# Performance work log

Hardware: AMD Instinct MI355X
Metric: run time of the kernel (lower is better)

Reference implementation:

```python
import jax, jax.numpy as jnp
import numpy as np

N1 = 10000; N2 = 10000; F_IN = 256
E_EDGES = 480000; P_PAIRS = 200000
HID = 128; H = 8; DH = 16; L = 2


def _segment_softmax(logits, seg, n):
    # softmax over edges sharing the same destination node (per head)
    m = jax.ops.segment_max(logits, seg, num_segments=n)
    m = jnp.where(jnp.isfinite(m), m, 0.0)
    e = jnp.exp(logits - m[seg])
    s = jax.ops.segment_sum(e, seg, num_segments=n)
    return e / (s[seg] + 1e-16)


def _attend(q_dst, k_src, v_src, src, dst, arel, mrel, prior, n_dst):
    # q_dst: [Nd,H,D]; k_src/v_src: [Ns,H,D]; arel/mrel: [H,D,D]; prior: [H]
    k = jnp.einsum('nhd,hde->nhe', k_src, arel)[src]   # [E,H,D]
    v = jnp.einsum('nhd,hde->nhe', v_src, mrel)[src]   # [E,H,D]
    logits = jnp.einsum('ehd,ehd->eh', q_dst[dst], k) * prior / jnp.sqrt(jnp.asarray(DH, q_dst.dtype))
    a = _segment_softmax(logits, dst, n_dst)           # [E,H]
    out = jax.ops.segment_sum(a[..., None] * v, dst, num_segments=n_dst)
    return out.reshape(n_dst, HID)


def _forward(x_n1, x_n2, Win1, bin1, Win2, bin2, Wk, bk, Wq, bq, Wv, bv, Wa, ba, skip, arel, mrel, prior, ei12, ei21, edge_index):
    proj = lambda x, W, b: (x @ W + b).reshape(-1, H, DH)
    h1 = jax.nn.relu(x_n1 @ Win1 + bin1)
    h2 = jax.nn.relu(x_n2 @ Win2 + bin2)
    feats1, feats2 = [], []
    for l in range(L):
        k1, q1, v1 = proj(h1, Wk[l, 0], bk[l, 0]), proj(h1, Wq[l, 0], bq[l, 0]), proj(h1, Wv[l, 0], bv[l, 0])
        k2, q2, v2 = proj(h2, Wk[l, 1], bk[l, 1]), proj(h2, Wq[l, 1], bq[l, 1]), proj(h2, Wv[l, 1], bv[l, 1])
        # edge type 0: n1 -> n2 (dst = n2); edge type 1: n2 -> n1 (dst = n1)
        agg2 = _attend(q2, k1, v1, ei12[0], ei12[1], arel[l, 0], mrel[l, 0], prior[l, 0], N2)
        agg1 = _attend(q1, k2, v2, ei21[0], ei21[1], arel[l, 1], mrel[l, 1], prior[l, 1], N1)
        o1 = jax.nn.gelu(agg1) @ Wa[l, 0] + ba[l, 0]
        o2 = jax.nn.gelu(agg2) @ Wa[l, 1] + ba[l, 1]
        s1 = jax.nn.sigmoid(skip[l, 0]); s2 = jax.nn.sigmoid(skip[l, 1])
        h1 = s1 * o1 + (1.0 - s1) * h1
        h2 = s2 * o2 + (1.0 - s2) * h2
        feats1.append(h1); feats2.append(h2)
    Em = jnp.concatenate(feats1, axis=1)   # [N1, HID*L]
    Ed = jnp.concatenate(feats2, axis=1)   # [N2, HID*L]
    # scores = Em @ Ed.T then gather at (m_index, d_index); computed as gathered dot
    # products (same math, avoids [N1,N2] materialization). Dropout in eval mode.
    preds = jnp.einsum('pc,pc->p', Em[edge_index[0]], Ed[edge_index[1]])[:, None]
    return preds


def setup_inputs():
    key = jax.random.key(0)
    ks = jax.random.split(key, 16)
    sc = 0.05
    inp = {}
    inp['x_n1'] = jax.random.normal(ks[0], (N1, F_IN), jnp.float32)
    inp['x_n2'] = jax.random.normal(ks[1], (N2, F_IN), jnp.float32)
    inp['ei12'] = jnp.stack([jax.random.randint(ks[2], (E_EDGES,), 0, N1),
                             jax.random.randint(ks[3], (E_EDGES,), 0, N2)])
    inp['ei21'] = jnp.stack([jax.random.randint(ks[4], (E_EDGES,), 0, N2),
                             jax.random.randint(ks[5], (E_EDGES,), 0, N1)])
    inp['edge_index'] = jnp.stack([jax.random.randint(ks[6], (P_PAIRS,), 0, N1),
                                   jax.random.randint(ks[7], (P_PAIRS,), 0, N2)])
    inp['Win1'] = jax.random.normal(ks[8], (F_IN, HID), jnp.float32) * sc
    inp['bin1'] = jnp.zeros((HID,), jnp.float32)
    inp['Win2'] = jax.random.normal(ks[9], (F_IN, HID), jnp.float32) * sc
    inp['bin2'] = jnp.zeros((HID,), jnp.float32)
    inp['Wk'] = jax.random.normal(ks[10], (L, 2, HID, HID), jnp.float32) * sc
    inp['bk'] = jnp.zeros((L, 2, HID), jnp.float32)
    inp['Wq'] = jax.random.normal(ks[11], (L, 2, HID, HID), jnp.float32) * sc
    inp['bq'] = jnp.zeros((L, 2, HID), jnp.float32)
    inp['Wv'] = jax.random.normal(ks[12], (L, 2, HID, HID), jnp.float32) * sc
    inp['bv'] = jnp.zeros((L, 2, HID), jnp.float32)
    inp['Wa'] = jax.random.normal(ks[13], (L, 2, HID, HID), jnp.float32) * sc
    inp['ba'] = jnp.zeros((L, 2, HID), jnp.float32)
    inp['skip'] = jnp.ones((L, 2), jnp.float32)
    inp['arel'] = jax.random.normal(ks[14], (L, 2, H, DH, DH), jnp.float32) * 0.25
    inp['mrel'] = jax.random.normal(ks[15], (L, 2, H, DH, DH), jnp.float32) * 0.25
    inp['prior'] = jnp.ones((L, 2, H), jnp.float32)
    return inp


def reference(x_n1, x_n2, ei12, ei21, edge_index, Win1, bin1, Win2, bin2, Wk, bk, Wq, bq, Wv, bv, Wa, ba, skip, arel, mrel, prior):
    return _forward(x_n1, x_n2, Win1, bin1, Win2, bin2, Wk, bk, Wq, bq, Wv, bv, Wa, ba, skip, arel, mrel, prior, ei12, ei21, edge_index)
```

## Files before the change

### kernel.cpp

```cpp
#include <hip/hip_runtime.h>
#include <math.h>

#define N1c 10000
#define N2c 10000
#define F_INc 256
#define Ec 480000
#define Pc 200000
#define Lc 2
#define NPART 32
#define NPc 313
#define NBLK 256
#define CAPE 17408
#define CAPP 7936

using short8 = __attribute__((ext_vector_type(8))) short;
using float4v = __attribute__((ext_vector_type(4))) float;
using floatx2 = __attribute__((ext_vector_type(2))) float;

__device__ __forceinline__ float gelu_f(float x) {
    const float k0 = 0.7978845608028654f;
    const float k1 = 0.044715f;
    float x3 = x * x * x;
    float t = tanhf(k0 * (x + k1 * x3));
    return 0.5f * x * (1.0f + t);
}

__device__ __forceinline__ float bf2f(unsigned short x) {
    union { unsigned int u; float f; } c;
    c.u = ((unsigned int)x) << 16;
    return c.f;
}
__device__ __forceinline__ unsigned short f2bf(float f) {
    union { float f; unsigned int u; } c;
    c.f = f;
    unsigned int u = c.u;
    unsigned int r = (u + 0x7FFFu + ((u >> 16) & 1u)) >> 16;
    return (unsigned short)r;
}
__device__ __forceinline__ unsigned char f2fp8(float v) {
    unsigned int p = __builtin_amdgcn_cvt_pk_fp8_f32(v, v, 0u, false);
    return (unsigned char)(p & 0xFF);
}

__global__ __launch_bounds__(256) void prep_kernel(
    const float* __restrict__ Wq, const float* __restrict__ bq,
    const float* __restrict__ Wk, const float* __restrict__ bk,
    const float* __restrict__ Wv, const float* __restrict__ bv,
    const float* __restrict__ arel, const float* __restrict__ mrel,
    const float* __restrict__ prior,
    const float* __restrict__ Win1, const float* __restrict__ Win2,
    const float* __restrict__ Wa,
    short* __restrict__ Wqkvt, float* __restrict__ bqkv,
    short* __restrict__ Wint1, short* __restrict__ Wint2, short* __restrict__ Wat)
{
    int id = blockIdx.x * 256 + threadIdx.x;
    if (id < 196608) {
        int lt = id / 49152;
        int r = id - lt * 49152;
        int col = r >> 7, c = r & 127;
        short* Wout = Wqkvt + (size_t)lt * 384 * 128;
        float* bout = bqkv + lt * 384;
        if (col < 128) {
            Wout[col * 128 + c] = (short)f2bf(Wq[lt * 16384 + c * 128 + col]);
            if (c == 0) bout[col] = bq[lt * 128 + col];
            return;
        }
        int which = (col < 256) ? 0 : 1;
        int he = col - (which ? 256 : 128);
        int h = he >> 4, e = he & 15;
        const float* W = (which == 0 ? Wk : Wv) + lt * 16384;
        const float* b = (which == 0 ? bk : bv) + lt * 128;
        const float* R = (which == 0 ? arel : mrel) + lt * 2048;
        float sc = (which == 0) ? prior[lt * 8 + h] * 0.25f : 1.0f;
        float acc = 0.f;
        #pragma unroll
        for (int d = 0; d < 16; d++)
            acc += W[c * 128 + h * 16 + d] * R[(h * 16 + d) * 16 + e];
        Wout[col * 128 + c] = (short)f2bf(acc * sc);
        if (c == 0) {
            float bacc = 0.f;
            #pragma unroll
            for (int d = 0; d < 16; d++)
                bacc += b[h * 16 + d] * R[(h * 16 + d) * 16 + e];
            bout[col] = bacc * sc;
        }
    } else {
        int wid = id - 196608;
        if (wid < 65536) {
            int y = wid >> 15;
            int id2 = wid & 32767;
            int n = id2 >> 8, k = id2 & 255;
            const float* W = y ? Win2 : Win1;
            short* O = y ? Wint2 : Wint1;
            O[n * 256 + k] = (short)f2bf(W[k * 128 + n]);
        } else {
            int wid2 = wid - 65536;
            int lt = wid2 >> 14;
            int id2 = wid2 & 16383;
            int n = id2 >> 7, k = id2 & 127;
            Wat[lt * 16384 + n * 128 + k] = (short)f2bf(Wa[lt * 16384 + k * 128 + n]);
        }
    }
}

__global__ __launch_bounds__(256) void scatter_bins_kernel(
    const int* __restrict__ ei12, const int* __restrict__ ei21, const int* __restrict__ eidx,
    int* __restrict__ gcnt,
    unsigned int* __restrict__ stg12, unsigned int* __restrict__ stg21,
    unsigned int* __restrict__ stgm)
{
    int blk = blockIdx.x, z = blockIdx.y, t = threadIdx.x;
    const int* key; const int* pay; int E; unsigned int* stg; int cap;
    if (z == 0)      { key = ei12 + Ec; pay = ei12; E = Ec; stg = stg12; cap = CAPE; }
    else if (z == 1) { key = ei21 + Ec; pay = ei21; E = Ec; stg = stg21; cap = CAPE; }
    else             { key = eidx;      pay = nullptr; E = Pc; stg = stgm; cap = CAPP; }
    int chunk = (E + NBLK - 1) / NBLK;
    int start = blk * chunk;
    int stop = min(start + chunk, E);
    __shared__ int cnt[NPART];
    __shared__ int base[NPART];
    __shared__ int fill[NPART];
    if (t < NPART) cnt[t] = 0;
    __syncthreads();
    for (int e = start + t; e < stop; e += 256)
        atomicAdd(&cnt[key[e] / NPc], 1);
    __syncthreads();
    if (t < NPART) {
        base[t] = cnt[t] ? atomicAdd(&gcnt[z * NPART + t], cnt[t]) : 0;
        fill[t] = 0;
    }
    __syncthreads();
    for (int e = start + t; e < stop; e += 256) {
        unsigned int k = (unsigned int)key[e];
        int p = (int)(k / NPc);
        int r = atomicAdd(&fill[p], 1);
        unsigned int pk = (z == 2) ? ((k << 18) | (unsigned int)e)
                                   : ((k << 14) | (unsigned int)pay[e]);
        stg[(size_t)p * cap + base[p] + r] = pk;
    }
}

__global__ __launch_bounds__(256) void build_csr_kernel(
    const int* __restrict__ gcnt,
    const unsigned int* __restrict__ stg12, const unsigned int* __restrict__ stg21,
    const unsigned int* __restrict__ stgm,
    int* __restrict__ rp12, int* __restrict__ rp21, int* __restrict__ rpm,
    int* __restrict__ es12, int* __restrict__ es21, int* __restrict__ ps)
{
    int p = blockIdx.x, z = blockIdx.y, t = threadIdx.x;
    const unsigned int* stg; int* rowptr; int* out; int cap;
    if (z == 0)      { stg = stg12; rowptr = rp12; out = es12; cap = CAPE; }
    else if (z == 1) { stg = stg21; rowptr = rp21; out = es21; cap = CAPE; }
    else             { stg = stgm;  rowptr = rpm;  out = ps;   cap = CAPP; }
    int ksh = (z == 2) ? 18 : 14;
    unsigned int pmask = (z == 2) ? 0x3FFFFu : 0x3FFFu;
    int baseOut = 0, cntP = 0;
    #pragma unroll
    for (int j = 0; j < NPART; j++) {
        int c = gcnt[z * NPART + j];
        if (j < p) baseOut += c;
        if (j == p) cntP = c;
    }
    const unsigned int* sbase = stg + (size_t)p * cap;
    int lo = p * NPc;
    int hi = min(lo + NPc, 10000);

    __shared__ int hist[512];
    __shared__ int fill[NPc];
    hist[t] = 0; hist[t + 256] = 0;
    __syncthreads();
    for (int i = t; i < cntP; i += 256)
        atomicAdd(&hist[(int)(sbase[i] >> ksh) - lo], 1);
    __syncthreads();
    for (int off = 1; off < 512; off <<= 1) {
        int i0 = t, i1 = t + 256;
        int v0 = (i0 >= off) ? hist[i0 - off] : 0;
        int v1 = (i1 >= off) ? hist[i1 - off] : 0;
        __syncthreads();
        hist[i0] += v0; hist[i1] += v1;
        __syncthreads();
    }
    for (int i = t; i < NPc; i += 256) {
        int excl = i ? hist[i - 1] : 0;
        fill[i] = excl;
        if (lo + i < hi) rowptr[lo + i] = baseOut + excl;
    }
    if (p == NPART - 1 && t == 0) rowptr[10000] = baseOut + cntP;
    __syncthreads();
    for (int i = t; i < cntP; i += 256) {
        unsigned int pk = sbase[i];
        int r = atomicAdd(&fill[(int)(pk >> ksh) - lo], 1);
        out[baseOut + r] = (int)(pk & pmask);
    }
}

template<int A_GELU, int OUT_RELU, int SKIP, int PACKQKV, int ABF, int KT>
__global__ __launch_bounds__(256) void gemm_mfma(
    const void* __restrict__ A0v, const void* __restrict__ A1v, int ldA,
    const short* __restrict__ Wt0, const short* __restrict__ Wt1,
    const float* __restrict__ b0, const float* __restrict__ b1,
    unsigned short* __restrict__ C0, unsigned short* __restrict__ C1, int ldC,
    unsigned char* __restrict__ KV8o0, unsigned char* __restrict__ KV8o1,
    int M,
    const float* __restrict__ sk0, const float* __restrict__ sk1,
    const unsigned short* __restrict__ H0, const unsigned short* __restrict__ H1, int ldH)
{
    int z = blockIdx.z;
    const void* Av = z ? A1v : A0v;
    const short* Wt = z ? Wt1 : Wt0;
    const float* bias = z ? b1 : b0;
    unsigned short* C = z ? C1 : C0;
    unsigned char* KV8o = z ? KV8o1 : KV8o0;
    const float* skipv = z ? sk1 : sk0;
    const unsigned short* Hold = z ? H1 : H0;

    __shared__ short Alds[64 * 40];
    __shared__ short Blds[64 * 40];

    int tid = threadIdx.x;
    int w = tid >> 6;
    int l = tid & 63;
    int mBase = blockIdx.x * 64;
    int nBase = blockIdx.y * 64;

    int srow = tid >> 2;
    int koct = tid & 3;

    float4v acc[4];
    #pragma unroll
    for (int i = 0; i < 4; i++) acc[i] = (float4v){0.f, 0.f, 0.f, 0.f};

    int arow = mBase + srow;
    const short* Wptr = Wt + (size_t)(nBase + srow) * KT + koct * 8;

    int fl = l & 15;
    int fo = (l >> 4) * 8;

    #pragma unroll
    for (int k0 = 0; k0 < KT; k0 += 32) {
        uint4 raw;
        if (ABF) {
            const unsigned short* Ab = (const unsigned short*)Av;
            raw = make_uint4(0u, 0u, 0u, 0u);
            if (arow < M) raw = *(const uint4*)(Ab + (size_t)arow * ldA + k0 + koct * 8);
            if (A_GELU) {
                unsigned int wd[4] = {raw.x, raw.y, raw.z, raw.w};
                #pragma unroll
                for (int i = 0; i < 4; i++) {
                    float lo = gelu_f(bf2f((unsigned short)(wd[i] & 0xFFFFu)));
                    float hi = gelu_f(bf2f((unsigned short)(wd[i] >> 16)));
                    wd[i] = (unsigned int)f2bf(lo) | ((unsigned int)f2bf(hi) << 16);
                }
                raw = make_uint4(wd[0], wd[1], wd[2], wd[3]);
            }
        } else {
            const float* Af = (const float*)Av;
            float av[8];
            if (arow < M) {
                const float4* p = (const float4*)(Af + (size_t)arow * ldA + k0 + koct * 8);
                float4 f0 = p[0], f1 = p[1];
                av[0]=f0.x; av[1]=f0.y; av[2]=f0.z; av[3]=f0.w;
                av[4]=f1.x; av[5]=f1.y; av[6]=f1.z; av[7]=f1.w;
            } else {
                #pragma unroll
                for (int i = 0; i < 8; i++) av[i] = 0.f;
            }
            unsigned int pk[4];
            #pragma unroll
            for (int i = 0; i < 4; i++)
                pk[i] = (unsigned int)f2bf(av[2*i]) | ((unsigned int)f2bf(av[2*i+1]) << 16);
            raw = make_uint4(pk[0], pk[1], pk[2], pk[3]);
        }
        *(uint4*)&Alds[srow * 40 + koct * 8] = raw;
        *(uint4*)&Blds[srow * 40 + koct * 8] = *(const uint4*)(Wptr + k0);
        __syncthreads();

        short8 bfr = *(const short8*)&Blds[(w * 16 + fl) * 40 + fo];
        #pragma unroll
        for (int msub = 0; msub < 4; msub++) {
            short8 afr = *(const short8*)&Alds[(msub * 16 + fl) * 40 + fo];
            acc[msub] = __builtin_amdgcn_mfma_f32_16x16x32_bf16(afr, bfr, acc[msub], 0, 0, 0);
        }
        __syncthreads();
    }

    float sig = 0.f;
    if (SKIP) sig = 1.f / (1.f + __expf(-skipv[0]));
    int col = nBase + w * 16 + fl;
    float bcol = bias[col];
    int rbase = mBase + ((l >> 4) * 4);
    #pragma unroll
    for (int msub = 0; msub < 4; msub++) {
        #pragma unroll
        for (int r = 0; r < 4; r++) {
            int row = rbase + msub * 16 + r;
            if (row >= M) continue;
            float v = acc[msub][r] + bcol;
            if (OUT_RELU) v = fmaxf(v, 0.f);
            if (SKIP) v = sig * v + (1.f - sig) * bf2f(Hold[(size_t)row * ldH + col]);
            if (PACKQKV) {
                if (col < 128) {
                    C[(size_t)row * ldC + col] = f2bf(v);
                } else if (col < 256) {
                    int c = col - 128;
                    KV8o[(size_t)row * 256 + (c >> 3) * 16 + (c & 7)] = f2fp8(v);
                } else {
                    int c = col - 256;
                    KV8o[(size_t)row * 256 + (c >> 3) * 16 + 8 + (c & 7)] = f2fp8(v);
                }
            } else {
                C[(size_t)row * ldC + col] = f2bf(v);
            }
        }
    }
}

__global__ __launch_bounds__(128) void attend_kernel(
    const unsigned short* __restrict__ Qb1, const unsigned char* __restrict__ KV81,
    const unsigned short* __restrict__ Qb2, const unsigned char* __restrict__ KV82,
    const int* __restrict__ rp12, const int* __restrict__ es12,
    const int* __restrict__ rp21, const int* __restrict__ es21,
    unsigned short* __restrict__ agg1, unsigned short* __restrict__ agg2)
{
    int b = blockIdx.x;
    const unsigned short* Qb; const unsigned char* KV; const int* rp; const int* es;
    unsigned short* outb; int n;
    if (b < 1250) { n = b * 8 + (threadIdx.x >> 4);          Qb = Qb2; KV = KV81; rp = rp12; es = es12; outb = agg2; }
    else          { n = (b - 1250) * 8 + (threadIdx.x >> 4); Qb = Qb1; KV = KV82; rp = rp21; es = es21; outb = agg1; }
    int ln = threadIdx.x & 15;

    float q[8];
    {
        const ushort4* qp = (const ushort4*)(Qb + (size_t)n * 128 + 8 * ln);
        ushort4 qa = qp[0], qc = qp[1];
        q[0]=bf2f(qa.x); q[1]=bf2f(qa.y); q[2]=bf2f(qa.z); q[3]=bf2f(qa.w);
        q[4]=bf2f(qc.x); q[5]=bf2f(qc.y); q[6]=bf2f(qc.z); q[7]=bf2f(qc.w);
    }
    int beg = rp[n], end = rp[n + 1];
    float s = 0.f;
    float acc[8];
    #pragma unroll
    for (int c = 0; c < 8; c++) acc[c] = 0.f;

    auto dec8 = [&](unsigned int w0, unsigned int w1, float* d) {
        floatx2 a0 = __builtin_amdgcn_cvt_pk_f32_fp8(w0, false);
        floatx2 a1 = __builtin_amdgcn_cvt_pk_f32_fp8(w0, true);
        floatx2 a2 = __builtin_amdgcn_cvt_pk_f32_fp8(w1, false);
        floatx2 a3 = __builtin_amdgcn_cvt_pk_f32_fp8(w1, true);
        d[0]=a0[0]; d[1]=a0[1]; d[2]=a1[0]; d[3]=a1[1];
        d[4]=a2[0]; d[5]=a2[1]; d[6]=a3[0]; d[7]=a3[1];
    };
    auto proc1 = [&](uint4 kv) {
        float kd[8], vd[8];
        dec8(kv.x, kv.y, kd);
        float p = q[0]*kd[0] + q[1]*kd[1] + q[2]*kd[2] + q[3]*kd[3]
                + q[4]*kd[4] + q[5]*kd[5] + q[6]*kd[6] + q[7]*kd[7];
        p += __shfl_xor(p, 1, 2);
        float x = __expf(p);
        s += x;
        dec8(kv.z, kv.w, vd);
        #pragma unroll
        for (int c = 0; c < 8; c++) acc[c] += x * vd[c];
    };
    auto ld = [&](int e) { return *(const uint4*)(KV + (size_t)e * 256 + 16 * ln); };

    int i = beg;
    int pre = min(end, (beg + 3) & ~3);
    for (; i < pre; i++) proc1(ld(es[i]));
    for (; i + 8 <= end; i += 8) {
        int4 ea = *(const int4*)&es[i];
        int4 eb = *(const int4*)&es[i + 4];
        uint4 w0 = ld(ea.x), w1 = ld(ea.y), w2 = ld(ea.z), w3 = ld(ea.w);
        uint4 w4 = ld(eb.x), w5 = ld(eb.y), w6 = ld(eb.z), w7 = ld(eb.w);
        proc1(w0); proc1(w1); proc1(w2); proc1(w3);
        proc1(w4); proc1(w5); proc1(w6); proc1(w7);
    }
    for (; i + 4 <= end; i += 4) {
        int4 ea = *(const int4*)&es[i];
        uint4 w0 = ld(ea.x), w1 = ld(ea.y), w2 = ld(ea.z), w3 = ld(ea.w);
        proc1(w0); proc1(w1); proc1(w2); proc1(w3);
    }
    for (; i < end; i++) proc1(ld(es[i]));

    float inv = 1.f / (s + 1e-16f);
    unsigned int w0 = (unsigned int)f2bf(acc[0]*inv) | ((unsigned int)f2bf(acc[1]*inv) << 16);
    unsigned int w1 = (unsigned int)f2bf(acc[2]*inv) | ((unsigned int)f2bf(acc[3]*inv) << 16);
    unsigned int w2 = (unsigned int)f2bf(acc[4]*inv) | ((unsigned int)f2bf(acc[5]*inv) << 16);
    unsigned int w3 = (unsigned int)f2bf(acc[6]*inv) | ((unsigned int)f2bf(acc[7]*inv) << 16);
    *(uint4*)(outb + (size_t)n * 128 + 8 * ln) = make_uint4(w0, w1, w2, w3);
}

__global__ __launch_bounds__(256) void pred_kernel(
    const unsigned short* __restrict__ Emb, const unsigned short* __restrict__ Edb,
    const int* __restrict__ eidx,
    const int* __restrict__ rpm, const int* __restrict__ porder,
    float* __restrict__ out)
{
    int m = blockIdx.x * 4 + (threadIdx.x >> 6);
    int lane = threadIdx.x & 63;
    int beg = rpm[m], end = rpm[m + 1];
    if (beg == end) return;
    ushort4 au = *(const ushort4*)(Emb + (size_t)m * 256 + 4 * lane);
    float4 a = make_float4(bf2f(au.x), bf2f(au.y), bf2f(au.z), bf2f(au.w));
    int i = beg;
    for (; i + 2 <= end; i += 2) {
        int p0 = porder[i], p1 = porder[i + 1];
        int d0 = eidx[Pc + p0], d1 = eidx[Pc + p1];
        ushort4 u0 = *(const ushort4*)(Edb + (size_t)d0 * 256 + 4 * lane);
        ushort4 u1 = *(const ushort4*)(Edb + (size_t)d1 * 256 + 4 * lane);
        float s0 = a.x*bf2f(u0.x) + a.y*bf2f(u0.y) + a.z*bf2f(u0.z) + a.w*bf2f(u0.w);
        float s1 = a.x*bf2f(u1.x) + a.y*bf2f(u1.y) + a.z*bf2f(u1.z) + a.w*bf2f(u1.w);
        #pragma unroll
        for (int o = 1; o < 64; o <<= 1) { s0 += __shfl_xor(s0, o); s1 += __shfl_xor(s1, o); }
        if (lane == 0) { out[p0] = s0; out[p1] = s1; }
    }
    if (i < end) {
        int p0 = porder[i];
        int d0 = eidx[Pc + p0];
        ushort4 u0 = *(const ushort4*)(Edb + (size_t)d0 * 256 + 4 * lane);
        float s0 = a.x*bf2f(u0.x) + a.y*bf2f(u0.y) + a.z*bf2f(u0.z) + a.w*bf2f(u0.w);
        #pragma unroll
        for (int o = 1; o < 64; o <<= 1) s0 += __shfl_xor(s0, o);
        if (lane == 0) out[p0] = s0;
    }
}

extern "C" void kernel_launch(void* const* d_in, const int* in_sizes, int n_in,
                              void* d_out, int out_size, void* d_ws, size_t ws_size,
                              hipStream_t stream)
{
    const float* x1   = (const float*)d_in[0];
    const float* x2   = (const float*)d_in[1];
    const int*   ei12 = (const int*)d_in[2];
    const int*   ei21 = (const int*)d_in[3];
    const int*   eidx = (const int*)d_in[4];
    const float* Win1 = (const float*)d_in[5];
    const float* bin1 = (const float*)d_in[6];
    const float* Win2 = (const float*)d_in[7];
    const float* bin2 = (const float*)d_in[8];
    const float* Wk   = (const float*)d_in[9];
    const float* bk   = (const float*)d_in[10];
    const float* Wq   = (const float*)d_in[11];
    const float* bq   = (const float*)d_in[12];
    const float* Wv   = (const float*)d_in[13];
    const float* bv   = (const float*)d_in[14];
    const float* Wa   = (const float*)d_in[15];
    const float* ba   = (const float*)d_in[16];
    const float* skip = (const float*)d_in[17];
    const float* arel = (const float*)d_in[18];
    const float* mrel = (const float*)d_in[19];
    const float* prior= (const float*)d_in[20];

    char* ws = (char*)d_ws;
    size_t off = 0;
    auto allocB = [&](size_t bytes) { void* p = ws + off; off += (bytes + 15) & ~15ull; return p; };
    auto allocF = [&](size_t n) { return (float*)allocB(n * 4); };
    auto allocI = [&](size_t n) { return (int*)allocB(n * 4); };
    auto allocS = [&](size_t n) { return (short*)allocB(n * 2); };
    auto allocU = [&](size_t n) { return (unsigned short*)allocB(n * 2); };

    unsigned short* h1b  = allocU((size_t)N1c * 128);
    unsigned short* h2b  = allocU((size_t)N2c * 128);
    unsigned short* Qb1  = allocU((size_t)N1c * 128);
    unsigned short* Qb2  = allocU((size_t)N2c * 128);
    unsigned char*  KV81 = (unsigned char*)allocB((size_t)N1c * 256);
    unsigned char*  KV82 = (unsigned char*)allocB((size_t)N2c * 256);
    unsigned short* agg1 = allocU((size_t)N1c * 128);
    unsigned short* agg2 = allocU((size_t)N2c * 128);
    unsigned short* Emb  = allocU((size_t)N1c * 256);
    unsigned short* Edb  = allocU((size_t)N2c * 256);
    float* bqkv  = allocF(4 * 384);
    short* Wqkvt = allocS(4 * 384 * 128);
    short* Wint1 = allocS(128 * 256);
    short* Wint2 = allocS(128 * 256);
    short* Wat   = allocS(4 * 128 * 128);
    int* rp12  = allocI(N2c + 1);
    int* rp21  = allocI(N1c + 1);
    int* rpm   = allocI(N1c + 1);
    int* es12  = allocI(Ec);
    int* es21  = allocI(Ec);
    int* ps    = allocI(Pc);
    int* gcnt  = allocI(3 * NPART);
    unsigned int* stg12 = (unsigned int*)allocB((size_t)NPART * CAPE * 4);
    unsigned int* stg21 = (unsigned int*)allocB((size_t)NPART * CAPE * 4);
    unsigned int* stgm  = (unsigned int*)allocB((size_t)NPART * CAPP * 4);

    hipMemsetAsync(gcnt, 0, 3 * NPART * sizeof(int), stream);

    prep_kernel<<<1280, 256, 0, stream>>>(
        Wq, bq, Wk, bk, Wv, bv, arel, mrel, prior,
        Win1, Win2, Wa, Wqkvt, bqkv, Wint1, Wint2, Wat);

    scatter_bins_kernel<<<dim3(NBLK, 3), 256, 0, stream>>>(
        ei12, ei21, eidx, gcnt, stg12, stg21, stgm);
    build_csr_kernel<<<dim3(NPART, 3), 256, 0, stream>>>(
        gcnt, stg12, stg21, stgm, rp12, rp21, rpm, es12, es21, ps);

    const int MB = (N1c + 63) / 64;
    gemm_mfma<0, 1, 0, 0, 0, 256><<<dim3(MB, 2, 2), 256, 0, stream>>>(
        x1, x2, F_INc, Wint1, Wint2, bin1, bin2, h1b, h2b, 128,
        nullptr, nullptr,
        N1c, nullptr, nullptr, nullptr, nullptr, 0);

    for (int l = 0; l < Lc; l++) {
        const unsigned short* A1 = (l == 0) ? h1b : Emb;  int ld1 = (l == 0) ? 128 : 256;
        const unsigned short* A2 = (l == 0) ? h2b : Edb;
        int lt0 = l * 2 + 0, lt1 = l * 2 + 1;
        gemm_mfma<0, 0, 0, 1, 1, 128><<<dim3(MB, 6, 2), 256, 0, stream>>>(
            A1, A2, ld1,
            Wqkvt + (size_t)lt0 * 49152, Wqkvt + (size_t)lt1 * 49152,
            bqkv + lt0 * 384, bqkv + lt1 * 384,
            Qb1, Qb2, 128,
            KV81, KV82,
            N1c, nullptr, nullptr, nullptr, nullptr, 0);
        attend_kernel<<<(N1c + N2c) / 8, 128, 0, stream>>>(
            Qb1, KV81, Qb2, KV82, rp12, es12, rp21, es21, agg1, agg2);
        gemm_mfma<1, 0, 1, 0, 1, 128><<<dim3(MB, 2, 2), 256, 0, stream>>>(
            agg1, agg2, 128,
            Wat + (size_t)lt0 * 16384, Wat + (size_t)lt1 * 16384,
            ba + lt0 * 128, ba + lt1 * 128,
            Emb + l * 128, Edb + l * 128, 256,
            nullptr, nullptr,
            N1c,
            skip + lt0, skip + lt1,
            A1, A2, ld1);
    }

    pred_kernel<<<N1c / 4, 256, 0, stream>>>(Emb, Edb, eidx, rpm, ps, (float*)d_out);
}
```

Before: 318.3 us.

## Fuse consecutive GEMMs via LDS-resident hidden tile and widen pred dot-product parallelism

Chains the input/output projection GEMM with the following QKV projection in one kernel. The 64-row hidden tile stays in LDS (Hlds) and feeds the second MFMA GEMM directly, so the intermediate is not re-read from global memory and two launches are saved. A separate gemm_out_kernel handles the final layer's output projection. The pred kernel now processes four pairs per wavefront, with 16 lanes each doing 16-element dot products, instead of a full-wave reduction per pair. The trade-off is a much larger LDS footprint (about 62KB) and high accumulator register use (acc2 is 6x4 float4 per thread), with grids of only about 314 blocks, which may hurt occupancy.

```diff
diff --git a/kernel.cpp b/kernel.cpp
--- a/kernel.cpp
+++ b/kernel.cpp
@@ -194,65 +194,68 @@
     }
 }
 
-template<int A_GELU, int OUT_RELU, int SKIP, int PACKQKV, int ABF, int KT>
-__global__ __launch_bounds__(256) void gemm_mfma(
+template<int MODE>
+__global__ __launch_bounds__(256) void gemm_fused(
     const void* __restrict__ A0v, const void* __restrict__ A1v, int ldA,
-    const short* __restrict__ Wt0, const short* __restrict__ Wt1,
-    const float* __restrict__ b0, const float* __restrict__ b1,
-    unsigned short* __restrict__ C0, unsigned short* __restrict__ C1, int ldC,
-    unsigned char* __restrict__ KV8o0, unsigned char* __restrict__ KV8o1,
-    int M,
+    const short* __restrict__ W1t0, const short* __restrict__ W1t1,
+    const float* __restrict__ b10, const float* __restrict__ b11,
+    unsigned short* __restrict__ H0o, unsigned short* __restrict__ H1o, int ldHo,
+    const unsigned short* __restrict__ Hold0, const unsigned short* __restrict__ Hold1, int ldHold,
     const float* __restrict__ sk0, const float* __restrict__ sk1,
-    const unsigned short* __restrict__ H0, const unsigned short* __restrict__ H1, int ldH)
-{
+    const short* __restrict__ W2t0, const short* __restrict__ W2t1,
+    const float* __restrict__ b20, const float* __restrict__ b21,
+    unsigned short* __restrict__ Qb0o, unsigned short* __restrict__ Qb1o,
+    unsigned char* __restrict__ KV80o, unsigned char* __restrict__ KV81o,
+    int M)
+{
+    const int KT = MODE ? 128 : 256;
     int z = blockIdx.z;
     const void* Av = z ? A1v : A0v;
-    const short* Wt = z ? Wt1 : Wt0;
-    const float* bias = z ? b1 : b0;
-    unsigned short* C = z ? C1 : C0;
-    unsigned char* KV8o = z ? KV8o1 : KV8o0;
+    const short* W1 = z ? W1t1 : W1t0;
+    const float* b1 = z ? b11 : b10;
+    unsigned short* Ho = z ? H1o : H0o;
+    const unsigned short* Hold = z ? Hold1 : Hold0;
     const float* skipv = z ? sk1 : sk0;
-    const unsigned short* Hold = z ? H1 : H0;
-
-    __shared__ short Alds[64 * 40];
-    __shared__ short Blds[64 * 40];
+    const short* W2 = z ? W2t1 : W2t0;
+    const float* b2 = z ? b21 : b20;
+    unsigned short* Qbo = z ? Qb1o : Qb0o;
+    unsigned char* KV8o = z ? KV81o : KV80o;
+
+    __shared__ short smem[31744];
+    short* Alds  = smem;
+    short* Blds1 = smem + 2560;
+    short* Hlds  = smem + 7680;
+    short* Blds2 = smem + 16384;
 
     int tid = threadIdx.x;
-    int w = tid >> 6;
-    int l = tid & 63;
+    int w = tid >> 6, l = tid & 63;
     int mBase = blockIdx.x * 64;
-    int nBase = blockIdx.y * 64;
-
-    int srow = tid >> 2;
-    int koct = tid & 3;
-
-    float4v acc[4];
-    #pragma unroll
-    for (int i = 0; i < 4; i++) acc[i] = (float4v){0.f, 0.f, 0.f, 0.f};
-
+    int srow = tid >> 2, koct = tid & 3;
+    int fl = l & 15, fo = (l >> 4) * 8;
     int arow = mBase + srow;
-    const short* Wptr = Wt + (size_t)(nBase + srow) * KT + koct * 8;
-
-    int fl = l & 15;
-    int fo = (l >> 4) * 8;
+    int rbase = mBase + ((l >> 4) * 4);
+
+    float4v acc1[2][4];
+    #pragma unroll
+    for (int s = 0; s < 2; s++)
+        #pragma unroll
+        for (int i = 0; i < 4; i++) acc1[s][i] = (float4v){0.f, 0.f, 0.f, 0.f};
 
     #pragma unroll
     for (int k0 = 0; k0 < KT; k0 += 32) {
         uint4 raw;
-        if (ABF) {
+        if (MODE) {
             const unsigned short* Ab = (const unsigned short*)Av;
             raw = make_uint4(0u, 0u, 0u, 0u);
             if (arow < M) raw = *(const uint4*)(Ab + (size_t)arow * ldA + k0 + koct * 8);
-            if (A_GELU) {
-                unsigned int wd[4] = {raw.x, raw.y, raw.z, raw.w};
-                #pragma unroll
-                for (int i = 0; i < 4; i++) {
-                    float lo = gelu_f(bf2f((unsigned short)(wd[i] & 0xFFFFu)));
-                    float hi = gelu_f(bf2f((unsigned short)(wd[i] >> 16)));
-                    wd[i] = (unsigned int)f2bf(lo) | ((unsigned int)f2bf(hi) << 16);
-                }
-                raw = make_uint4(wd[0], wd[1], wd[2], wd[3]);
+            unsigned int wd[4] = {raw.x, raw.y, raw.z, raw.w};
+            #pragma unroll
+            for (int i = 0; i < 4; i++) {
+                float lo = gelu_f(bf2f((unsigned short)(wd[i] & 0xFFFFu)));
+                float hi = gelu_f(bf2f((unsigned short)(wd[i] >> 16)));
+                wd[i] = (unsigned int)f2bf(lo) | ((unsigned int)f2bf(hi) << 16);
             }
+            raw = make_uint4(wd[0], wd[1], wd[2], wd[3]);
         } else {
             const float* Af = (const float*)Av;
             float av[8];
@@ -272,35 +275,86 @@
             raw = make_uint4(pk[0], pk[1], pk[2], pk[3]);
         }
         *(uint4*)&Alds[srow * 40 + koct * 8] = raw;
-        *(uint4*)&Blds[srow * 40 + koct * 8] = *(const uint4*)(Wptr + k0);
-        __syncthreads();
-
-        short8 bfr = *(const short8*)&Blds[(w * 16 + fl) * 40 + fo];
+        #pragma unroll
+        for (int r = 0; r < 2; r++) {
+            int n = srow + 64 * r;
+            *(uint4*)&Blds1[n * 40 + koct * 8] = *(const uint4*)(W1 + (size_t)n * KT + k0 + koct * 8);
+        }
+        __syncthreads();
+        #pragma unroll
+        for (int s = 0; s < 2; s++) {
+            short8 bfr = *(const short8*)&Blds1[(s * 64 + w * 16 + fl) * 40 + fo];
+            #pragma unroll
+            for (int msub = 0; msub < 4; msub++) {
+                short8 afr = *(const short8*)&Alds[(msub * 16 + fl) * 40 + fo];
+                acc1[s][msub] = __builtin_amdgcn_mfma_f32_16x16x32_bf16(afr, bfr, acc1[s][msub], 0, 0, 0);
+            }
+        }
+        __syncthreads();
+    }
+
+    float sig = 0.f;
+    if (MODE) sig = 1.f / (1.f + __expf(-skipv[0]));
+    #pragma unroll
+    for (int s = 0; s < 2; s++) {
+        int col = s * 64 + w * 16 + fl;
+        float bc = b1[col];
         #pragma unroll
         for (int msub = 0; msub < 4; msub++) {
-            short8 afr = *(const short8*)&Alds[(msub * 16 + fl) * 40 + fo];
-            acc[msub] = __builtin_amdgcn_mfma_f32_16x16x32_bf16(afr, bfr, acc[msub], 0, 0, 0);
-        }
-        __syncthreads();
-    }
-
-    float sig = 0.f;
-    if (SKIP) sig = 1.f / (1.f + __expf(-skipv[0]));
-    int col = nBase + w * 16 + fl;
-    float bcol = bias[col];
-    int rbase = mBase + ((l >> 4) * 4);
-    #pragma unroll
-    for (int msub = 0; msub < 4; msub++) {
-        #pragma unroll
-        for (int r = 0; r < 4; r++) {
-            int row = rbase + msub * 16 + r;
-            if (row >= M) continue;
-            float v = acc[msub][r] + bcol;
-            if (OUT_RELU) v = fmaxf(v, 0.f);
-            if (SKIP) v = sig * v + (1.f - sig) * bf2f(Hold[(size_t)row * ldH + col]);
-            if (PACKQKV) {
+            #pragma unroll
+            for (int r = 0; r < 4; r++) {
+                int row = rbase + msub * 16 + r;
+                if (row >= M) continue;
+                float v = acc1[s][msub][r] + bc;
+                if (MODE) v = sig * v + (1.f - sig) * bf2f(Hold[(size_t)row * ldHold + col]);
+                else v = fmaxf(v, 0.f);
+                unsigned short hb = f2bf(v);
+                Ho[(size_t)row * ldHo + col] = hb;
+                Hlds[(row - mBase) * 136 + col] = (short)hb;
+            }
+        }
+    }
+    __syncthreads();
+
+    float4v acc2[6][4];
+    #pragma unroll
+    for (int s = 0; s < 6; s++)
+        #pragma unroll
+        for (int i = 0; i < 4; i++) acc2[s][i] = (float4v){0.f, 0.f, 0.f, 0.f};
+
+    #pragma unroll
+    for (int k0 = 0; k0 < 128; k0 += 32) {
+        #pragma unroll
+        for (int r = 0; r < 6; r++) {
+            int n = srow + 64 * r;
+            *(uint4*)&Blds2[n * 40 + koct * 8] = *(const uint4*)(W2 + (size_t)n * 128 + k0 + koct * 8);
+        }
+        __syncthreads();
+        #pragma unroll
+        for (int s = 0; s < 6; s++) {
+            short8 bfr = *(const short8*)&Blds2[(w * 96 + s * 16 + fl) * 40 + fo];
+            #pragma unroll
+            for (int msub = 0; msub < 4; msub++) {
+                short8 afr = *(const short8*)&Hlds[(msub * 16 + fl) * 136 + k0 + fo];
+                acc2[s][msub] = __builtin_amdgcn_mfma_f32_16x16x32_bf16(afr, bfr, acc2[s][msub], 0, 0, 0);
+            }
+        }
+        __syncthreads();
+    }
+
+    #pragma unroll
+    for (int s = 0; s < 6; s++) {
+        int col = w * 96 + s * 16 + fl;
+        float bc = b2[col];
+        #pragma unroll
+        for (int msub = 0; msub < 4; msub++) {
+            #pragma unroll
+            for (int r = 0; r < 4; r++) {
+                int row = rbase + msub * 16 + r;
+                if (row >= M) continue;
+                float v = acc2[s][msub][r] + bc;
                 if (col < 128) {
-                    C[(size_t)row * ldC + col] = f2bf(v);
+                    Qbo[(size_t)row * 128 + col] = f2bf(v);
                 } else if (col < 256) {
                     int c = col - 128;
                     KV8o[(size_t)row * 256 + (c >> 3) * 16 + (c & 7)] = f2fp8(v);
@@ -308,9 +362,79 @@
                     int c = col - 256;
                     KV8o[(size_t)row * 256 + (c >> 3) * 16 + 8 + (c & 7)] = f2fp8(v);
                 }
-            } else {
-                C[(size_t)row * ldC + col] = f2bf(v);
             }
+        }
+    }
+}
+
+__global__ __launch_bounds__(256) void gemm_out_kernel(
+    const unsigned short* __restrict__ A0, const unsigned short* __restrict__ A1,
+    const short* __restrict__ Wt0, const short* __restrict__ Wt1,
+    const float* __restrict__ b0, const float* __restrict__ b1,
+    unsigned short* __restrict__ C0, unsigned short* __restrict__ C1,
+    const float* __restrict__ sk0, const float* __restrict__ sk1,
+    const unsigned short* __restrict__ H0, const unsigned short* __restrict__ H1,
+    int M)
+{
+    int z = blockIdx.z;
+    const unsigned short* A = z ? A1 : A0;
+    const short* Wt = z ? Wt1 : Wt0;
+    const float* bias = z ? b1 : b0;
+    unsigned short* C = z ? C1 : C0;
+    const float* skipv = z ? sk1 : sk0;
+    const unsigned short* Hold = z ? H1 : H0;
+
+    __shared__ short Alds[64 * 40];
+    __shared__ short Blds[64 * 40];
+
+    int tid = threadIdx.x;
+    int w = tid >> 6, l = tid & 63;
+    int mBase = blockIdx.x * 64;
+    int nBase = blockIdx.y * 64;
+    int srow = tid >> 2, koct = tid & 3;
+    int fl = l & 15, fo = (l >> 4) * 8;
+    int arow = mBase + srow;
+
+    float4v acc[4];
+    #pragma unroll
+    for (int i = 0; i < 4; i++) acc[i] = (float4v){0.f, 0.f, 0.f, 0.f};
+
+    #pragma unroll
+    for (int k0 = 0; k0 < 128; k0 += 32) {
+        uint4 raw = make_uint4(0u, 0u, 0u, 0u);
+        if (arow < M) raw = *(const uint4*)(A + (size_t)arow * 128 + k0 + koct * 8);
+        unsigned int wd[4] = {raw.x, raw.y, raw.z, raw.w};
+        #pragma unroll
+        for (int i = 0; i < 4; i++) {
+            float lo = gelu_f(bf2f((unsigned short)(wd[i] & 0xFFFFu)));
+            float hi = gelu_f(bf2f((unsigned short)(wd[i] >> 16)));
+            wd[i] = (unsigned int)f2bf(lo) | ((unsigned int)f2bf(hi) << 16);
+        }
+        *(uint4*)&Alds[srow * 40 + koct * 8] = make_uint4(wd[0], wd[1], wd[2], wd[3]);
+        *(uint4*)&Blds[srow * 40 + koct * 8] = *(const uint4*)(Wt + (size_t)(nBase + srow) * 128 + k0 + koct * 8);
+        __syncthreads();
+        short8 bfr = *(const short8*)&Blds[(w * 16 + fl) * 40 + fo];
+        #pragma unroll
+        for (int msub = 0; msub < 4; msub++) {
+            short8 afr = *(const short8*)&Alds[(msub * 16 + fl) * 40 + fo];
+            acc[msub] = __builtin_amdgcn_mfma_f32_16x16x32_bf16(afr, bfr, acc[msub], 0, 0, 0);
+        }
+        __syncthreads();
+    }
+
+    float sig = 1.f / (1.f + __expf(-skipv[0]));
+    int col = nBase + w * 16 + fl;
+    float bcol = bias[col];
+    int rbase = mBase + ((l >> 4) * 4);
+    #pragma unroll
+    for (int msub = 0; msub < 4; msub++) {
+        #pragma unroll
+        for (int r = 0; r < 4; r++) {
+            int row = rbase + msub * 16 + r;
+            if (row >= M) continue;
+            float v = acc[msub][r] + bcol;
+            v = sig * v + (1.f - sig) * bf2f(Hold[(size_t)row * 256 + col]);
+            C[(size_t)row * 256 + col] = f2bf(v);
         }
     }
 }
@@ -397,31 +521,38 @@
     float* __restrict__ out)
 {
     int m = blockIdx.x * 4 + (threadIdx.x >> 6);
-    int lane = threadIdx.x & 63;
+    int l = threadIdx.x & 63;
+    int g = l >> 4;
+    int ln = l & 15;
     int beg = rpm[m], end = rpm[m + 1];
     if (beg == end) return;
-    ushort4 au = *(const ushort4*)(Emb + (size_t)m * 256 + 4 * lane);
-    float4 a = make_float4(bf2f(au.x), bf2f(au.y), bf2f(au.z), bf2f(au.w));
-    int i = beg;
-    for (; i + 2 <= end; i += 2) {
-        int p0 = porder[i], p1 = porder[i + 1];
-        int d0 = eidx[Pc + p0], d1 = eidx[Pc + p1];
-        ushort4 u0 = *(const ushort4*)(Edb + (size_t)d0 * 256 + 4 * lane);
-        ushort4 u1 = *(const ushort4*)(Edb + (size_t)d1 * 256 + 4 * lane);
-        float s0 = a.x*bf2f(u0.x) + a.y*bf2f(u0.y) + a.z*bf2f(u0.z) + a.w*bf2f(u0.w);
-        float s1 = a.x*bf2f(u1.x) + a.y*bf2f(u1.y) + a.z*bf2f(u1.z) + a.w*bf2f(u1.w);
-        #pragma unroll
-        for (int o = 1; o < 64; o <<= 1) { s0 += __shfl_xor(s0, o); s1 += __shfl_xor(s1, o); }
-        if (lane == 0) { out[p0] = s0; out[p1] = s1; }
-    }
-    if (i < end) {
-        int p0 = porder[i];
-        int d0 = eidx[Pc + p0];
-        ushort4 u0 = *(const ushort4*)(Edb + (size_t)d0 * 256 + 4 * lane);
-        float s0 = a.x*bf2f(u0.x) + a.y*bf2f(u0.y) + a.z*bf2f(u0.z) + a.w*bf2f(u0.w);
-        #pragma unroll
-        for (int o = 1; o < 64; o <<= 1) s0 += __shfl_xor(s0, o);
-        if (lane == 0) out[p0] = s0;
+    float a[16];
+    {
+        const uint4* ap = (const uint4*)(Emb + (size_t)m * 256 + 16 * ln);
+        uint4 u0 = ap[0], u1 = ap[1];
+        unsigned int wv[8] = {u0.x, u0.y, u0.z, u0.w, u1.x, u1.y, u1.z, u1.w};
+        #pragma unroll
+        for (int i = 0; i < 8; i++) {
+            a[2*i]   = bf2f((unsigned short)(wv[i] & 0xFFFFu));
+            a[2*i+1] = bf2f((unsigned short)(wv[i] >> 16));
+        }
+    }
+    for (int i = beg + g; i < end; i += 4) {
+        int p = porder[i];
+        int d = eidx[Pc + p];
+        const uint4* bp = (const uint4*)(Edb + (size_t)d * 256 + 16 * ln);
+        uint4 u0 = bp[0], u1 = bp[1];
+        unsigned int wv[8] = {u0.x, u0.y, u0.z, u0.w, u1.x, u1.y, u1.z, u1.w};
+        float s = 0.f;
+        #pragma unroll
+        for (int j = 0; j < 8; j++)
+            s += a[2*j] * bf2f((unsigned short)(wv[j] & 0xFFFFu))
+               + a[2*j+1] * bf2f((unsigned short)(wv[j] >> 16));
+        s += __shfl_xor(s, 1, 16);
+        s += __shfl_xor(s, 2, 16);
+        s += __shfl_xor(s, 4, 16);
+        s += __shfl_xor(s, 8, 16);
+        if (ln == 0) out[p] = s;
     }
 }
 
@@ -497,34 +628,37 @@
         gcnt, stg12, stg21, stgm, rp12, rp21, rpm, es12, es21, ps);
 
     const int MB = (N1c + 63) / 64;
-    gemm_mfma<0, 1, 0, 0, 0, 256><<<dim3(MB, 2, 2), 256, 0, stream>>>(
-        x1, x2, F_INc, Wint1, Wint2, bin1, bin2, h1b, h2b, 128,
-        nullptr, nullptr,
-        N1c, nullptr, nullptr, nullptr, nullptr, 0);
-
-    for (int l = 0; l < Lc; l++) {
-        const unsigned short* A1 = (l == 0) ? h1b : Emb;  int ld1 = (l == 0) ? 128 : 256;
-        const unsigned short* A2 = (l == 0) ? h2b : Edb;
-        int lt0 = l * 2 + 0, lt1 = l * 2 + 1;
-        gemm_mfma<0, 0, 0, 1, 1, 128><<<dim3(MB, 6, 2), 256, 0, stream>>>(
-            A1, A2, ld1,
-            Wqkvt + (size_t)lt0 * 49152, Wqkvt + (size_t)lt1 * 49152,
-            bqkv + lt0 * 384, bqkv + lt1 * 384,
-            Qb1, Qb2, 128,
-            KV81, KV82,
-            N1c, nullptr, nullptr, nullptr, nullptr, 0);
-        attend_kernel<<<(N1c + N2c) / 8, 128, 0, stream>>>(
-            Qb1, KV81, Qb2, KV82, rp12, es12, rp21, es21, agg1, agg2);
-        gemm_mfma<1, 0, 1, 0, 1, 128><<<dim3(MB, 2, 2), 256, 0, stream>>>(
-            agg1, agg2, 128,
-            Wat + (size_t)lt0 * 16384, Wat + (size_t)lt1 * 16384,
-            ba + lt0 * 128, ba + lt1 * 128,
-            Emb + l * 128, Edb + l * 128, 256,
-            nullptr, nullptr,
-            N1c,
-            skip + lt0, skip + lt1,
-            A1, A2, ld1);
-    }
+
+    gemm_fused<0><<<dim3(MB, 1, 2), 256, 0, stream>>>(
+        x1, x2, F_INc,
+        Wint1, Wint2, bin1, bin2,
+        h1b, h2b, 128,
+        nullptr, nullptr, 0, nullptr, nullptr,
+        Wqkvt + 0 * 49152, Wqkvt + 1 * 49152,
+        bqkv + 0 * 384, bqkv + 1 * 384,
+        Qb1, Qb2, KV81, KV82, N1c);
+
+    attend_kernel<<<(N1c + N2c) / 8, 128, 0, stream>>>(
+        Qb1, KV81, Qb2, KV82, rp12, es12, rp21, es21, agg1, agg2);
+
+    gemm_fused<1><<<dim3(MB, 1, 2), 256, 0, stream>>>(
+        agg1, agg2, 128,
+        Wat + 0 * 16384, Wat + 1 * 16384, ba + 0 * 128, ba + 1 * 128,
+        Emb, Edb, 256,
+        h1b, h2b, 128, skip + 0, skip + 1,
+        Wqkvt + 2 * 49152, Wqkvt + 3 * 49152,
+        bqkv + 2 * 384, bqkv + 3 * 384,
+        Qb1, Qb2, KV81, KV82, N1c);
+
+    attend_kernel<<<(N1c + N2c) / 8, 128, 0, stream>>>(
+        Qb1, KV81, Qb2, KV82, rp12, es12, rp21, es21, agg1, agg2);
+
+    gemm_out_kernel<<<dim3(MB, 2, 2), 256, 0, stream>>>(
+        agg1, agg2,
+        Wat + 2 * 16384, Wat + 3 * 16384, ba + 2 * 128, ba + 3 * 128,
+        Emb + 128, Edb + 128,
+        skip + 2, skip + 3,
+        Emb, Edb, N1c);
 
     pred_kernel<<<N1c / 4, 256, 0, stream>>>(Emb, Edb, eidx, rpm, ps, (float*)d_out);
 }
```

Result: slower. 330.1 us (+3.7%).
